# Kernel optimization log

Hardware: AMD Instinct MI355X
Metric: run time of the kernel (lower is better)

Reference implementation:

```python
import jax, jax.numpy as jnp
import numpy as np

DIM = 1024
CTX_DIM = 1024
VALUE_DIM = 1024
HEADS = 16
HEAD_DIM = DIM // HEADS        # q/k head dim = 64
V_HEAD_DIM = VALUE_DIM // HEADS
LN_EPS = 1e-5


def setup_inputs() -> dict:
    key = jax.random.key(0)
    k0, k1, k2, k3, k4 = jax.random.split(key, 5)
    B, N, M = 4, 1024, 1024
    x = jax.random.normal(k0, (B, N, DIM), jnp.float32)
    context = jax.random.normal(k1, (B, M, CTX_DIM), jnp.float32)
    # Linear weights stored as [in, out] (y = x @ W), matching torch Linear math
    Wq = jax.random.normal(k2, (DIM, DIM), jnp.float32) * (DIM ** -0.5)
    Wkv = jax.random.normal(k3, (CTX_DIM, DIM + VALUE_DIM), jnp.float32) * (CTX_DIM ** -0.5)
    Wt = jax.random.normal(k4, (HEADS, HEADS), jnp.float32) * (HEADS ** -0.5)
    gamma = jnp.ones((HEADS,), jnp.float32)
    beta = jnp.zeros((HEADS,), jnp.float32)
    return {"x": x, "context": context, "Wq": Wq, "Wkv": Wkv,
            "Wt": Wt, "gamma": gamma, "beta": beta}


def reference(x, context, Wq, Wkv, Wt, gamma, beta):
    B, N, _ = x.shape
    M = context.shape[1]
    # projections
    q = (x @ Wq).reshape(B, N, HEADS, HEAD_DIM).transpose(0, 2, 1, 3)       # [B,H,N,d]
    kv = context @ Wkv                                                      # [B,M,dim+vdim]
    k = kv[..., :DIM].reshape(B, M, HEADS, HEAD_DIM).transpose(0, 2, 1, 3)  # [B,H,M,d]
    v = kv[..., DIM:].reshape(B, M, HEADS, V_HEAD_DIM).transpose(0, 2, 1, 3)
    # scaled dot-product scores, fully materialized as in the original
    scale = HEAD_DIM ** -0.5
    dots = jnp.einsum('bhid,bhjd->bhij', q * scale, k)                      # [B,H,N,M]
    w = jax.nn.softmax(dots, axis=-1)
    # talking heads: Linear(heads,heads,bias=False) then LayerNorm(heads) over head axis
    w = jnp.einsum('bhij,hg->bgij', w, Wt)
    mu = jnp.mean(w, axis=1, keepdims=True)
    var = jnp.var(w, axis=1, keepdims=True)
    w = (w - mu) * jax.lax.rsqrt(var + LN_EPS)
    w = w * gamma[None, :, None, None] + beta[None, :, None, None]
    attn = jnp.einsum('bhij,bhjd->bhid', w, v)                              # [B,H,N,vd]
    out = attn.transpose(0, 2, 1, 3).reshape(B, N, VALUE_DIM)
    return out
```

## Files before the change

### kernel.cpp

```cpp
#include <hip/hip_runtime.h>
#include <hip/hip_bf16.h>

typedef __bf16 bf16;
typedef bf16 bf16x2 __attribute__((ext_vector_type(2)));
typedef bf16 bf16x4 __attribute__((ext_vector_type(4)));
typedef bf16 bf16x8 __attribute__((ext_vector_type(8)));
typedef float floatx4 __attribute__((ext_vector_type(4)));

#define MFMA_BF16(a, b, c) __builtin_amdgcn_mfma_f32_16x16x32_bf16((a), (b), (c), 0, 0, 0)

__global__ __launch_bounds__(256) void cvt2_kernel(const float* __restrict__ x,
                                                   const float* __restrict__ ctx,
                                                   bf16* __restrict__ xb,
                                                   bf16* __restrict__ cb) {
    int idx = blockIdx.x * 256 + threadIdx.x;
    const float* in;
    bf16* out;
    int i;
    if (idx < 524288) { in = x; out = xb; i = idx; }
    else              { in = ctx; out = cb; i = idx - 524288; }
    const float* src = in + (size_t)i * 8;
    float4 f0 = *(const float4*)src;
    float4 f1 = *(const float4*)(src + 4);
    bf16x8 v = {(bf16)f0.x, (bf16)f0.y, (bf16)f0.z, (bf16)f0.w,
                (bf16)f1.x, (bf16)f1.y, (bf16)f1.z, (bf16)f1.w};
    *(bf16x8*)(out + (size_t)i * 8) = v;
}

__global__ __launch_bounds__(256) void trans2_kernel(const float* __restrict__ Wq,
                                                     const float* __restrict__ Wkv,
                                                     bf16* __restrict__ WqT,
                                                     bf16* __restrict__ WkvT) {
    const int z = blockIdx.z;
    if (z == 0 && blockIdx.x >= 32) return;
    const float* in = z ? Wkv : Wq;
    bf16* out = z ? WkvT : WqT;
    const int C = z ? 2048 : 1024, R = 1024;
    __shared__ float tile[32][33];
    const int t = threadIdx.x;
    const int r0 = blockIdx.y * 32, c0 = blockIdx.x * 32;
    int r = t >> 3, c4 = (t & 7) * 4;
    float4 v = *(const float4*)&in[(size_t)(r0 + r) * C + c0 + c4];
    tile[r][c4 + 0] = v.x; tile[r][c4 + 1] = v.y;
    tile[r][c4 + 2] = v.z; tile[r][c4 + 3] = v.w;
    __syncthreads();
    int rp = t >> 3, cp = (t & 7) * 4;
    bf16x4 w = {(bf16)tile[cp + 0][rp], (bf16)tile[cp + 1][rp],
                (bf16)tile[cp + 2][rp], (bf16)tile[cp + 3][rp]};
    *(bf16x4*)&out[(size_t)(c0 + rp) * R + r0 + cp] = w;
}

__global__ __launch_bounds__(256) void gemm_all(const bf16* __restrict__ xb,
                                                const bf16* __restrict__ cb,
                                                const bf16* __restrict__ WqT,
                                                const bf16* __restrict__ WkvT,
                                                bf16* __restrict__ Qb,
                                                bf16* __restrict__ Kb,
                                                bf16* __restrict__ Vt) {
    __shared__ bf16 As[128 * 40];
    __shared__ bf16 Bs[128 * 40];
    const bool isQ = blockIdx.x < 8;
    const bf16* A = isQ ? xb : cb;
    const bf16* B = isQ ? WqT : WkvT;
    const int t = threadIdx.x;
    const int wv = t >> 6, lane = t & 63, quad = lane >> 4, l15 = lane & 15;
    const int wr = wv >> 1, wc = wv & 1;
    const int m0 = blockIdx.y * 128;
    const int n0 = (isQ ? blockIdx.x : blockIdx.x - 8) * 128;
    const int ra = t >> 1, kc = (t & 1) * 16;

    floatx4 acc[4][4] = {};

    for (int k0 = 0; k0 < 1024; k0 += 32) {
        bf16x8 a0 = *(const bf16x8*)&A[(size_t)(m0 + ra) * 1024 + k0 + kc];
        bf16x8 a1 = *(const bf16x8*)&A[(size_t)(m0 + ra) * 1024 + k0 + kc + 8];
        bf16x8 b0 = *(const bf16x8*)&B[(size_t)(n0 + ra) * 1024 + k0 + kc];
        bf16x8 b1 = *(const bf16x8*)&B[(size_t)(n0 + ra) * 1024 + k0 + kc + 8];
        __syncthreads();
        *(bf16x8*)&As[ra * 40 + kc] = a0;
        *(bf16x8*)&As[ra * 40 + kc + 8] = a1;
        *(bf16x8*)&Bs[ra * 40 + kc] = b0;
        *(bf16x8*)&Bs[ra * 40 + kc + 8] = b1;
        __syncthreads();
        bf16x8 af[4], bfr[4];
#pragma unroll
        for (int mt = 0; mt < 4; ++mt)
            af[mt] = *(bf16x8*)&As[(wr * 64 + mt * 16 + l15) * 40 + quad * 8];
#pragma unroll
        for (int nt = 0; nt < 4; ++nt)
            bfr[nt] = *(bf16x8*)&Bs[(wc * 64 + nt * 16 + l15) * 40 + quad * 8];
#pragma unroll
        for (int mt = 0; mt < 4; ++mt)
#pragma unroll
            for (int nt = 0; nt < 4; ++nt)
                acc[mt][nt] = MFMA_BF16(af[mt], bfr[nt], acc[mt][nt]);
    }
#pragma unroll
    for (int mt = 0; mt < 4; ++mt)
#pragma unroll
        for (int nt = 0; nt < 4; ++nt) {
            int mb = m0 + wr * 64 + mt * 16 + quad * 4;
            int n = n0 + wc * 64 + nt * 16 + l15;
            if (isQ) {
#pragma unroll
                for (int r = 0; r < 4; ++r)
                    Qb[(size_t)(mb + r) * 1024 + n] = (bf16)acc[mt][nt][r];
            } else if (n < 1024) {
#pragma unroll
                for (int r = 0; r < 4; ++r)
                    Kb[(size_t)(mb + r) * 1024 + n] = (bf16)acc[mt][nt][r];
            } else {
                int nn = n - 1024, h = nn >> 6, d = nn & 63;
                int bb = mb >> 10, j = mb & 1023;
                bf16x4 v4 = {(bf16)acc[mt][nt][0], (bf16)acc[mt][nt][1],
                             (bf16)acc[mt][nt][2], (bf16)acc[mt][nt][3]};
                *(bf16x4*)&Vt[(size_t)((bb * 16 + h) * 64 + d) * 1024 + j] = v4;
            }
        }
}

__global__ __launch_bounds__(256) void denom_kernel(const bf16* __restrict__ Qb,
                                                    const bf16* __restrict__ Kb,
                                                    float* __restrict__ L) {
    const int t = threadIdx.x;
    const int wv = t >> 6, lane = t & 63, quad = lane >> 4, l15 = lane & 15;
    const int i0 = blockIdx.x * 32, b = blockIdx.y, jz = blockIdx.z;
    const float scale = 0.125f;
    const bf16* Kbase = Kb + (size_t)b * 1024 * 1024;

    for (int hh = 0; hh < 4; ++hh) {
        const int h = wv * 4 + hh;
        bf16x8 qa[2][2];
#pragma unroll
        for (int it = 0; it < 2; ++it) {
            const bf16* qp = Qb + (size_t)(b * 1024 + i0 + it * 16 + l15) * 1024 +
                             h * 64 + quad * 8;
            qa[it][0] = *(const bf16x8*)qp;
            qa[it][1] = *(const bf16x8*)(qp + 32);
        }
        floatx4 se[2] = {};
#pragma unroll
        for (int jt = 0; jt < 8; ++jt) {
            int j = jz * 128 + jt * 16 + l15;
            const bf16* kp = Kbase + (size_t)j * 1024 + h * 64 + quad * 8;
            bf16x8 k0 = *(const bf16x8*)kp;
            bf16x8 k1 = *(const bf16x8*)(kp + 32);
#pragma unroll
            for (int it = 0; it < 2; ++it) {
                floatx4 c = {0.f, 0.f, 0.f, 0.f};
                c = MFMA_BF16(qa[it][0], k0, c);
                c = MFMA_BF16(qa[it][1], k1, c);
#pragma unroll
                for (int r = 0; r < 4; ++r) se[it][r] += __expf(c[r] * scale);
            }
        }
#pragma unroll
        for (int it = 0; it < 2; ++it)
#pragma unroll
            for (int r = 0; r < 4; ++r) {
                float s = se[it][r];
                s += __shfl_xor(s, 1); s += __shfl_xor(s, 2);
                s += __shfl_xor(s, 4); s += __shfl_xor(s, 8);
                if (l15 == 0)
                    atomicAdd(&L[(size_t)(b * 16 + h) * 1024 + i0 + it * 16 +
                                 quad * 4 + r], s);
            }
    }
}

__global__ __launch_bounds__(512, 4) void attn_kernel(const bf16* __restrict__ Qb,
                                                      const bf16* __restrict__ Kb,
                                                      const bf16* __restrict__ Vt,
                                                      const float* __restrict__ L,
                                                      const float* __restrict__ Wt,
                                                      const float* __restrict__ gamma,
                                                      const float* __restrict__ beta,
                                                      float* __restrict__ out) {
    __shared__ bf16 Buf1[512 * 20];
    __shared__ bf16 Buf2[16 * 640];

    const int t = threadIdx.x;
    const int wv = t >> 6, lane = t & 63, quad = lane >> 4, l15 = lane & 15;
    const int i0 = blockIdx.x * 16, b = blockIdx.y, jz = blockIdx.z;
    const float scale = 0.125f;

    bf16x8 a_wt;
#pragma unroll
    for (int jj = 0; jj < 8; ++jj) {
        int k = quad * 8 + jj;
        float v = 0.f;
        if (k < 16) {
            float s = 0.f;
            for (int g = 0; g < 16; ++g) s += Wt[k * 16 + g];
            v = Wt[k * 16 + l15] - s * 0.0625f;
        }
        a_wt[jj] = (bf16)v;
    }
    float gq[4], bq[4];
#pragma unroll
    for (int r = 0; r < 4; ++r) { gq[r] = gamma[quad * 4 + r]; bq[r] = beta[quad * 4 + r]; }

    bf16x8 qa[2][2];
    float invl[2][4];
#pragma unroll
    for (int hh = 0; hh < 2; ++hh) {
        int h = wv * 2 + hh;
        const bf16* qp = Qb + (size_t)(b * 1024 + i0 + l15) * 1024 + h * 64 + quad * 8;
        qa[hh][0] = *(const bf16x8*)qp;
        qa[hh][1] = *(const bf16x8*)(qp + 32);
#pragma unroll
        for (int r = 0; r < 4; ++r)
            invl[hh][r] = 1.f / L[(size_t)(b * 16 + h) * 1024 + i0 + quad * 4 + r];
    }

    const bf16* Kbase = Kb + (size_t)b * 1024 * 1024;
    const bf16* Vbase = Vt + (size_t)b * 16 * 64 * 1024;
    floatx4 o[2][4] = {};

    for (int jt = 0; jt < 8; ++jt) {
        const int j0 = jz * 256 + jt * 32;
#pragma unroll
        for (int ns = 0; ns < 2; ++ns) {
            floatx4 cw[2];
#pragma unroll
            for (int hh = 0; hh < 2; ++hh) {
                int h = wv * 2 + hh;
                const bf16* kp = Kbase + (size_t)(j0 + ns * 16 + l15) * 1024 + h * 64 + quad * 8;
                floatx4 c = {0.f, 0.f, 0.f, 0.f};
                c = MFMA_BF16(qa[hh][0], *(const bf16x8*)kp, c);
                c = MFMA_BF16(qa[hh][1], *(const bf16x8*)(kp + 32), c);
                cw[hh] = c;
            }
#pragma unroll
            for (int r = 0; r < 4; ++r) {
                bf16x2 pk = {(bf16)(__expf(cw[0][r] * scale) * invl[0][r]),
                             (bf16)(__expf(cw[1][r] * scale) * invl[1][r])};
                *(bf16x2*)&Buf1[((quad * 4 + r) * 32 + ns * 16 + l15) * 20 + wv * 2] = pk;
            }
        }
        __syncthreads();
#pragma unroll
        for (int grp = 0; grp < 4; ++grp) {
            int gi = wv * 4 + grp, ig = gi >> 1, jb = (gi & 1) * 16;
            int p = ig * 32 + jb + l15;
            const bf16* src = &Buf1[p * 20 + (quad & 1) * 8];
            floatx4 c = {0.f, 0.f, 0.f, 0.f};
            c = MFMA_BF16(a_wt, *(const bf16x8*)src, c);
            float s2 = c[0] * c[0] + c[1] * c[1] + c[2] * c[2] + c[3] * c[3];
            s2 += __shfl_xor(s2, 16);
            s2 += __shfl_xor(s2, 32);
            float rs = rsqrtf(s2 * 0.0625f + 1e-5f);
#pragma unroll
            for (int r = 0; r < 4; ++r) {
                float w2 = c[r] * rs * gq[r] + bq[r];
                Buf2[(quad * 4 + r) * 640 + ig * 40 + jb + l15] = (bf16)w2;
            }
        }
        __syncthreads();
#pragma unroll
        for (int hh = 0; hh < 2; ++hh) {
            int g = wv * 2 + hh;
            bf16x8 a = *(bf16x8*)&Buf2[g * 640 + l15 * 40 + quad * 8];
#pragma unroll
            for (int dt = 0; dt < 4; ++dt) {
                const bf16* vp = Vbase + (size_t)(g * 64 + dt * 16 + l15) * 1024 +
                                 j0 + quad * 8;
                o[hh][dt] = MFMA_BF16(a, *(const bf16x8*)vp, o[hh][dt]);
            }
        }
    }
#pragma unroll
    for (int hh = 0; hh < 2; ++hh) {
        int g = wv * 2 + hh;
#pragma unroll
        for (int dt = 0; dt < 4; ++dt)
#pragma unroll
            for (int r = 0; r < 4; ++r)
                atomicAdd(&out[(size_t)(b * 1024 + i0 + quad * 4 + r) * 1024 +
                               g * 64 + dt * 16 + l15], o[hh][dt][r]);
    }
}

extern "C" void kernel_launch(void* const* d_in, const int* in_sizes, int n_in,
                              void* d_out, int out_size, void* d_ws, size_t ws_size,
                              hipStream_t stream) {
    const float* x     = (const float*)d_in[0];
    const float* ctx   = (const float*)d_in[1];
    const float* Wq    = (const float*)d_in[2];
    const float* Wkv   = (const float*)d_in[3];
    const float* Wt    = (const float*)d_in[4];
    const float* gamma = (const float*)d_in[5];
    const float* beta  = (const float*)d_in[6];
    float* out = (float*)d_out;

    bf16* xb   = (bf16*)d_ws;
    bf16* cb   = xb + (size_t)4 * 1024 * 1024;
    bf16* WqT  = cb + (size_t)4 * 1024 * 1024;
    bf16* WkvT = WqT + (size_t)1024 * 1024;
    bf16* Qb   = WkvT + (size_t)2048 * 1024;
    bf16* Kb   = Qb + (size_t)4 * 1024 * 1024;
    bf16* Vt   = Kb + (size_t)4 * 1024 * 1024;
    float* L   = (float*)(Vt + (size_t)4 * 1024 * 1024);

    hipMemsetAsync(L, 0, (size_t)4 * 16 * 1024 * sizeof(float), stream);
    hipMemsetAsync(out, 0, (size_t)out_size * sizeof(float), stream);

    cvt2_kernel<<<4096, 256, 0, stream>>>(x, ctx, xb, cb);
    trans2_kernel<<<dim3(64, 32, 2), 256, 0, stream>>>(Wq, Wkv, WqT, WkvT);
    gemm_all<<<dim3(24, 32), 256, 0, stream>>>(xb, cb, WqT, WkvT, Qb, Kb, Vt);
    denom_kernel<<<dim3(32, 4, 8), 256, 0, stream>>>(Qb, Kb, L);
    attn_kernel<<<dim3(64, 4, 4), 512, 0, stream>>>(Qb, Kb, Vt, L, Wt, gamma, beta, out);
}
```

Measured before the change: 365.6 us.

## Split attention into mix-weights materialization and separate PV GEMM kernel

```diff
diff --git a/kernel.cpp b/kernel.cpp
--- a/kernel.cpp
+++ b/kernel.cpp
@@ -168,117 +168,112 @@
     }
 }
 
-__global__ __launch_bounds__(512, 4) void attn_kernel(const bf16* __restrict__ Qb,
-                                                      const bf16* __restrict__ Kb,
-                                                      const bf16* __restrict__ Vt,
-                                                      const float* __restrict__ L,
-                                                      const float* __restrict__ Wt,
-                                                      const float* __restrict__ gamma,
-                                                      const float* __restrict__ beta,
-                                                      float* __restrict__ out) {
-    __shared__ bf16 Buf1[512 * 20];
-    __shared__ bf16 Buf2[16 * 640];
-
-    const int t = threadIdx.x;
+__global__ __launch_bounds__(256) void mixw_kernel(const bf16* __restrict__ Qb,
+                                                   const bf16* __restrict__ Kb,
+                                                   const float* __restrict__ L,
+                                                   const float* __restrict__ Wt,
+                                                   const float* __restrict__ gamma,
+                                                   const float* __restrict__ beta,
+                                                   bf16* __restrict__ Wf,
+                                                   int b_base, int g0, int gcnt) {
+    __shared__ float WtcLDS[256];
+    const int t = threadIdx.x;
+    {
+        int h = t >> 4, g = t & 15;
+        float s = 0.f;
+#pragma unroll
+        for (int gg = 0; gg < 16; ++gg) s += Wt[h * 16 + gg];
+        WtcLDS[t] = Wt[h * 16 + g] - s * 0.0625f;
+    }
+    __syncthreads();
+
     const int wv = t >> 6, lane = t & 63, quad = lane >> 4, l15 = lane & 15;
-    const int i0 = blockIdx.x * 16, b = blockIdx.y, jz = blockIdx.z;
+    const int task = blockIdx.x * 4 + wv;
+    const int jz = task & 7, it = (task >> 3) & 63, bl = task >> 9;
+    const int b = b_base + bl, i0 = it * 16;
     const float scale = 0.125f;
 
-    bf16x8 a_wt;
-#pragma unroll
-    for (int jj = 0; jj < 8; ++jj) {
-        int k = quad * 8 + jj;
-        float v = 0.f;
-        if (k < 16) {
-            float s = 0.f;
-            for (int g = 0; g < 16; ++g) s += Wt[k * 16 + g];
-            v = Wt[k * 16 + l15] - s * 0.0625f;
-        }
-        a_wt[jj] = (bf16)v;
-    }
-    float gq[4], bq[4];
-#pragma unroll
-    for (int r = 0; r < 4; ++r) { gq[r] = gamma[quad * 4 + r]; bq[r] = beta[quad * 4 + r]; }
-
-    bf16x8 qa[2][2];
-    float invl[2][4];
-#pragma unroll
-    for (int hh = 0; hh < 2; ++hh) {
-        int h = wv * 2 + hh;
-        const bf16* qp = Qb + (size_t)(b * 1024 + i0 + l15) * 1024 + h * 64 + quad * 8;
-        qa[hh][0] = *(const bf16x8*)qp;
-        qa[hh][1] = *(const bf16x8*)(qp + 32);
+    float invl[16];
+#pragma unroll
+    for (int h = 0; h < 16; ++h)
+        invl[h] = 1.f / L[(size_t)(b * 16 + h) * 1024 + i0 + l15];
+
+    const bf16* Qp0 = Qb + (size_t)(b * 1024 + i0 + l15) * 1024 + quad * 8;
+    const bf16* Kbase = Kb + (size_t)(b * 1024) * 1024 + quad * 8;
+
+    for (int jt = 0; jt < 8; ++jt) {
+        const int j0 = jz * 128 + jt * 16;
+        const bf16* Kp0 = Kbase + (size_t)(j0 + l15) * 1024;
+        floatx4 wmix[16];
+#pragma unroll
+        for (int g = 0; g < 16; ++g) wmix[g] = (floatx4){0.f, 0.f, 0.f, 0.f};
+
+        for (int h = 0; h < 16; ++h) {
+            bf16x8 aK0 = *(const bf16x8*)(Kp0 + h * 64);
+            bf16x8 aK1 = *(const bf16x8*)(Kp0 + h * 64 + 32);
+            bf16x8 bQ0 = *(const bf16x8*)(Qp0 + h * 64);
+            bf16x8 bQ1 = *(const bf16x8*)(Qp0 + h * 64 + 32);
+            floatx4 c = {0.f, 0.f, 0.f, 0.f};
+            c = MFMA_BF16(aK0, bQ0, c);
+            c = MFMA_BF16(aK1, bQ1, c);
+            floatx4 p;
+#pragma unroll
+            for (int r = 0; r < 4; ++r) p[r] = __expf(c[r] * scale) * invl[h];
+#pragma unroll
+            for (int g = 0; g < 16; ++g) {
+                float wc = WtcLDS[h * 16 + g];
+                wmix[g] += p * wc;
+            }
+        }
+        floatx4 s2 = {0.f, 0.f, 0.f, 0.f};
+#pragma unroll
+        for (int g = 0; g < 16; ++g) s2 += wmix[g] * wmix[g];
+        floatx4 rs;
+#pragma unroll
+        for (int r = 0; r < 4; ++r) rs[r] = rsqrtf(s2[r] * 0.0625f + 1e-5f);
+#pragma unroll
+        for (int g = 0; g < 16; ++g) {
+            if (g < g0 || g >= g0 + gcnt) continue;
+            float gm = gamma[g], bt = beta[g];
+            bf16x4 v;
+#pragma unroll
+            for (int r = 0; r < 4; ++r) v[r] = (bf16)(wmix[g][r] * rs[r] * gm + bt);
+            *(bf16x4*)&Wf[((size_t)((bl * gcnt + (g - g0)) * 1024 + i0 + l15)) * 1024 +
+                          j0 + quad * 4] = v;
+        }
+    }
+}
+
+__global__ __launch_bounds__(256) void pv_kernel(const bf16* __restrict__ Wf,
+                                                 const bf16* __restrict__ Vt,
+                                                 float* __restrict__ out,
+                                                 int b_base, int g0, int gshift) {
+    const int t = threadIdx.x;
+    const int wv = t >> 6, lane = t & 63, quad = lane >> 4, l15 = lane & 15;
+    const int gcnt = 1 << gshift;
+    const int task = blockIdx.x * 4 + wv;
+    const int it = task & 63, gl = (task >> 6) & (gcnt - 1), bl = task >> (6 + gshift);
+    const int b = b_base + bl, g = g0 + gl, i0 = it * 16;
+
+    const bf16* Wrow = Wf + ((size_t)((bl * gcnt + gl) * 1024 + i0 + l15)) * 1024 + quad * 8;
+    const bf16* Vbase = Vt + (size_t)((b * 16 + g) * 64) * 1024 + quad * 8;
+    floatx4 o[4] = {};
+
+    for (int c32 = 0; c32 < 32; ++c32) {
+        const int j0 = c32 * 32;
+        bf16x8 aW = *(const bf16x8*)(Wrow + j0);
+#pragma unroll
+        for (int dt = 0; dt < 4; ++dt) {
+            bf16x8 bV = *(const bf16x8*)(Vbase + (size_t)(dt * 16 + l15) * 1024 + j0);
+            o[dt] = MFMA_BF16(aW, bV, o[dt]);
+        }
+    }
+#pragma unroll
+    for (int dt = 0; dt < 4; ++dt)
 #pragma unroll
         for (int r = 0; r < 4; ++r)
-            invl[hh][r] = 1.f / L[(size_t)(b * 16 + h) * 1024 + i0 + quad * 4 + r];
-    }
-
-    const bf16* Kbase = Kb + (size_t)b * 1024 * 1024;
-    const bf16* Vbase = Vt + (size_t)b * 16 * 64 * 1024;
-    floatx4 o[2][4] = {};
-
-    for (int jt = 0; jt < 8; ++jt) {
-        const int j0 = jz * 256 + jt * 32;
-#pragma unroll
-        for (int ns = 0; ns < 2; ++ns) {
-            floatx4 cw[2];
-#pragma unroll
-            for (int hh = 0; hh < 2; ++hh) {
-                int h = wv * 2 + hh;
-                const bf16* kp = Kbase + (size_t)(j0 + ns * 16 + l15) * 1024 + h * 64 + quad * 8;
-                floatx4 c = {0.f, 0.f, 0.f, 0.f};
-                c = MFMA_BF16(qa[hh][0], *(const bf16x8*)kp, c);
-                c = MFMA_BF16(qa[hh][1], *(const bf16x8*)(kp + 32), c);
-                cw[hh] = c;
-            }
-#pragma unroll
-            for (int r = 0; r < 4; ++r) {
-                bf16x2 pk = {(bf16)(__expf(cw[0][r] * scale) * invl[0][r]),
-                             (bf16)(__expf(cw[1][r] * scale) * invl[1][r])};
-                *(bf16x2*)&Buf1[((quad * 4 + r) * 32 + ns * 16 + l15) * 20 + wv * 2] = pk;
-            }
-        }
-        __syncthreads();
-#pragma unroll
-        for (int grp = 0; grp < 4; ++grp) {
-            int gi = wv * 4 + grp, ig = gi >> 1, jb = (gi & 1) * 16;
-            int p = ig * 32 + jb + l15;
-            const bf16* src = &Buf1[p * 20 + (quad & 1) * 8];
-            floatx4 c = {0.f, 0.f, 0.f, 0.f};
-            c = MFMA_BF16(a_wt, *(const bf16x8*)src, c);
-            float s2 = c[0] * c[0] + c[1] * c[1] + c[2] * c[2] + c[3] * c[3];
-            s2 += __shfl_xor(s2, 16);
-            s2 += __shfl_xor(s2, 32);
-            float rs = rsqrtf(s2 * 0.0625f + 1e-5f);
-#pragma unroll
-            for (int r = 0; r < 4; ++r) {
-                float w2 = c[r] * rs * gq[r] + bq[r];
-                Buf2[(quad * 4 + r) * 640 + ig * 40 + jb + l15] = (bf16)w2;
-            }
-        }
-        __syncthreads();
-#pragma unroll
-        for (int hh = 0; hh < 2; ++hh) {
-            int g = wv * 2 + hh;
-            bf16x8 a = *(bf16x8*)&Buf2[g * 640 + l15 * 40 + quad * 8];
-#pragma unroll
-            for (int dt = 0; dt < 4; ++dt) {
-                const bf16* vp = Vbase + (size_t)(g * 64 + dt * 16 + l15) * 1024 +
-                                 j0 + quad * 8;
-                o[hh][dt] = MFMA_BF16(a, *(const bf16x8*)vp, o[hh][dt]);
-            }
-        }
-    }
-#pragma unroll
-    for (int hh = 0; hh < 2; ++hh) {
-        int g = wv * 2 + hh;
-#pragma unroll
-        for (int dt = 0; dt < 4; ++dt)
-#pragma unroll
-            for (int r = 0; r < 4; ++r)
-                atomicAdd(&out[(size_t)(b * 1024 + i0 + quad * 4 + r) * 1024 +
-                               g * 64 + dt * 16 + l15], o[hh][dt][r]);
-    }
+            out[(size_t)(b * 1024 + i0 + quad * 4 + r) * 1024 + g * 64 + dt * 16 + l15] =
+                o[dt][r];
 }
 
 extern "C" void kernel_launch(void* const* d_in, const int* in_sizes, int n_in,
@@ -293,21 +288,39 @@
     const float* beta  = (const float*)d_in[6];
     float* out = (float*)d_out;
 
+    const size_t MI = 1024 * 1024;
     bf16* xb   = (bf16*)d_ws;
-    bf16* cb   = xb + (size_t)4 * 1024 * 1024;
-    bf16* WqT  = cb + (size_t)4 * 1024 * 1024;
-    bf16* WkvT = WqT + (size_t)1024 * 1024;
-    bf16* Qb   = WkvT + (size_t)2048 * 1024;
-    bf16* Kb   = Qb + (size_t)4 * 1024 * 1024;
-    bf16* Vt   = Kb + (size_t)4 * 1024 * 1024;
-    float* L   = (float*)(Vt + (size_t)4 * 1024 * 1024);
-
-    hipMemsetAsync(L, 0, (size_t)4 * 16 * 1024 * sizeof(float), stream);
-    hipMemsetAsync(out, 0, (size_t)out_size * sizeof(float), stream);
+    bf16* cb   = xb + 4 * MI;
+    bf16* WqT  = cb + 4 * MI;
+    bf16* WkvT = WqT + 1 * MI;
+    bf16* Qb   = WkvT + 2 * MI;
+    bf16* Kb   = Qb + 4 * MI;
+    bf16* Vt   = Kb + 4 * MI;
+    float* L   = (float*)(Vt + 4 * MI);
+    bf16* Wf   = (bf16*)(L + 64 * 1024);
+
+    const size_t base_bytes = (size_t)23 * MI * 2 + 64 * 1024 * 4;
+
+    hipMemsetAsync(L, 0, (size_t)64 * 1024 * sizeof(float), stream);
 
     cvt2_kernel<<<4096, 256, 0, stream>>>(x, ctx, xb, cb);
     trans2_kernel<<<dim3(64, 32, 2), 256, 0, stream>>>(Wq, Wkv, WqT, WkvT);
     gemm_all<<<dim3(24, 32), 256, 0, stream>>>(xb, cb, WqT, WkvT, Qb, Kb, Vt);
     denom_kernel<<<dim3(32, 4, 8), 256, 0, stream>>>(Qb, Kb, L);
-    attn_kernel<<<dim3(64, 4, 4), 512, 0, stream>>>(Qb, Kb, Vt, L, Wt, gamma, beta, out);
-}
+
+    if (ws_size >= base_bytes + (size_t)64 * MI * 2) {
+        mixw_kernel<<<512, 256, 0, stream>>>(Qb, Kb, L, Wt, gamma, beta, Wf, 0, 0, 16);
+        pv_kernel<<<1024, 256, 0, stream>>>(Wf, Vt, out, 0, 0, 4);
+    } else if (ws_size >= base_bytes + (size_t)16 * MI * 2) {
+        for (int b = 0; b < 4; ++b) {
+            mixw_kernel<<<128, 256, 0, stream>>>(Qb, Kb, L, Wt, gamma, beta, Wf, b, 0, 16);
+            pv_kernel<<<256, 256, 0, stream>>>(Wf, Vt, out, b, 0, 4);
+        }
+    } else {
+        for (int b = 0; b < 4; ++b)
+            for (int gh = 0; gh < 16; gh += 8) {
+                mixw_kernel<<<128, 256, 0, stream>>>(Qb, Kb, L, Wt, gamma, beta, Wf, b, gh, 8);
+                pv_kernel<<<128, 256, 0, stream>>>(Wf, Vt, out, b, gh, 3);
+            }
+    }
+}
```

Measured after the change: 407.4 us. 1.11x slower.
